# Performance work log

Measured on AMD Instinct MI355X. Metric: run time of the kernel, lower is better.

The kernel has to match this reference:

```python
import jax, jax.numpy as jnp
import numpy as np

DIM = 1024
B, S = 2, 2048

def _gelu(v):
    return jax.nn.gelu(v, approximate=False)

def setup_inputs() -> dict:
    key = jax.random.key(0)
    ks = jax.random.split(key, 24)
    d = DIM
    def lin(k, fan_in, fan_out):
        k1, k2 = jax.random.split(k)
        bound = 1.0 / np.sqrt(fan_in)
        W = jax.random.uniform(k1, (fan_in, fan_out), jnp.float32, -bound, bound)
        b = jax.random.uniform(k2, (fan_out,), jnp.float32, -bound, bound)
        return W, b
    w_pt1, b_pt1 = lin(ks[0], d, 2 * d)
    w_pt2, b_pt2 = lin(ks[1], 2 * d, d)
    w_wg, b_wg = lin(ks[2], d, d)
    w_mag, b_mag = lin(ks[3], d, d)
    w_q1, b_q1 = lin(ks[4], d, d)
    w_q2, b_q2 = lin(ks[5], d, d)
    w_mix, b_mix = lin(ks[6], d, 2 * d)
    w_o1, b_o1 = lin(ks[7], d, d)
    w_o2, b_o2 = lin(ks[8], d, d)
    return {
        "x": jax.random.normal(ks[9], (B, S, d), jnp.float32),
        "w_pt1": w_pt1, "b_pt1": b_pt1, "w_pt2": w_pt2, "b_pt2": b_pt2,
        "int_scale": jnp.ones((d,), jnp.float32) * 0.001,
        "w_wg": w_wg, "b_wg": b_wg,
        "gate_temp": jnp.ones((1,), jnp.float32) * 2.0,
        "w_mag": w_mag, "b_mag": b_mag,
        "w_q1": w_q1, "b_q1": b_q1, "w_q2": w_q2, "b_q2": b_q2,
        "w_mix": w_mix, "b_mix": b_mix,
        "ln_g": jnp.ones((d,), jnp.float32), "ln_b": jnp.zeros((d,), jnp.float32),
        "w_o1": w_o1, "b_o1": b_o1, "w_o2": w_o2, "b_o2": b_o2,
    }

def reference(x, w_pt1, b_pt1, w_pt2, b_pt2, int_scale, w_wg, b_wg, gate_temp,
              w_mag, b_mag, w_q1, b_q1, w_q2, b_q2, w_mix, b_mix,
              ln_g, ln_b, w_o1, b_o1, w_o2, b_o2):
    # input-dependent phase basis
    phase_delta = _gelu(x @ w_pt1 + b_pt1) @ w_pt2 + b_pt2          # [B,S,D]
    phi = jnp.cumsum(phase_delta * jnp.abs(int_scale), axis=1)
    # selective write gate + magnitude
    write_gate = jax.nn.sigmoid((x @ w_wg + b_wg) * gate_temp)
    magnitude = jax.nn.sigmoid(x @ w_mag + b_mag) * 5.0
    content = write_gate * x * magnitude
    # complex-phase memory accumulation (4 seq-length scans)
    memory_real = jnp.cumsum(content * jnp.cos(phi), axis=1)
    memory_imag = jnp.cumsum(content * jnp.sin(phi), axis=1)
    accum_weight = jnp.cumsum(write_gate * magnitude + 1e-8, axis=1)
    inv_s = 1.0 / jnp.sqrt(accum_weight)
    mr, mi = memory_real * inv_s, memory_imag * inv_s
    # query-phase retrieval (complex rotation)
    query_phase = phi + (_gelu(x @ w_q1 + b_q1) @ w_q2 + b_q2)
    cq, sq = jnp.cos(query_phase), jnp.sin(query_phase)
    retrieved_real = mr * cq + mi * sq
    retrieved_imag = mi * cq - mr * sq
    # input-dependent output mixing
    mix = x @ w_mix + b_mix
    d = x.shape[-1]
    mix_real = jax.nn.sigmoid(mix[..., :d])
    mix_imag = jax.nn.sigmoid(mix[..., d:])
    retrieved = mix_real * retrieved_real + mix_imag * retrieved_imag
    # output head: LayerNorm -> Linear -> GELU -> (Dropout=identity in eval) -> Linear
    mu = jnp.mean(retrieved, axis=-1, keepdims=True)
    var = jnp.var(retrieved, axis=-1, keepdims=True)
    ln = (retrieved - mu) / jnp.sqrt(var + 1e-5) * ln_g + ln_b
    out = _gelu(ln @ w_o1 + b_o1) @ w_o2 + b_o2
    return x + out
```

## Files before the change

### kernel.cpp

```cpp
#include <hip/hip_runtime.h>
#include <hip/hip_bf16.h>

#define MTOT 4096
#define DD   1024
#define D2   2048
#define SS   2048
#define BB   2
#define NC2  128
#define CL2  (SS/NC2)

typedef __attribute__((ext_vector_type(8))) short bf16x8;
typedef __attribute__((ext_vector_type(4))) float f32x4;

__device__ __forceinline__ float sigmf(float v){
    return 1.0f/(1.0f+__expf(-v));
}
__device__ __forceinline__ float geluf(float v){
    float u = 0.7978845608f*v*(1.0f + 0.044715f*v*v);
    float e = __expf(2.0f*u);
    float t = 1.0f - 2.0f/(e + 1.0f);
    return 0.5f*v*(1.0f + t);
}
__device__ __forceinline__ ushort f2bf(float f){
    unsigned u = __float_as_uint(f);
    unsigned r = (u + 0x7FFF + ((u>>16)&1)) >> 16;
    return (ushort)r;
}
__device__ __forceinline__ float bf2f(ushort u){
    return __uint_as_float(((unsigned)u)<<16);
}

__device__ __forceinline__ void stage_tile(
    const ushort* __restrict__ A, const ushort* __restrict__ Bt, int K,
    int m0, int n0, int k0, ushort* As, ushort* Bs)
{
    int tid = threadIdx.x;
    #pragma unroll
    for (int i = 0; i < 2; i++) {
        int e = (i*256 + tid) * 8;
        int r = e >> 5;
        int s = (e >> 3) & 3;
        int c = ((s ^ ((r >> 1) & 3)) << 3);
        __builtin_amdgcn_global_load_lds(
            (const __attribute__((address_space(1))) void*)(A + (size_t)(m0 + r)*K + k0 + c),
            (__attribute__((address_space(3))) void*)(As + e), 16, 0, 0);
        __builtin_amdgcn_global_load_lds(
            (const __attribute__((address_space(1))) void*)(Bt + (size_t)(n0 + r)*K + k0 + c),
            (__attribute__((address_space(3))) void*)(Bs + e), 16, 0, 0);
    }
}

__device__ __forceinline__ void load_frags(
    const ushort* As, const ushort* Bs, int wr, int wc, int lrow, int cs,
    bf16x8 (&af)[4], bf16x8 (&bfr)[4])
{
    #pragma unroll
    for (int i = 0; i < 4; i++) {
        int ra = wr*64 + i*16 + lrow;
        int rb = wc*64 + i*16 + lrow;
        af[i]  = *(const bf16x8*)(As + ra*32 + ((cs ^ ((ra>>1)&3))<<3));
        bfr[i] = *(const bf16x8*)(Bs + rb*32 + ((cs ^ ((rb>>1)&3))<<3));
    }
}

__device__ __forceinline__ void do_mfma(
    const bf16x8 (&af)[4], const bf16x8 (&bfr)[4], f32x4 (&acc)[4][4])
{
    __builtin_amdgcn_s_setprio(1);
    #pragma unroll
    for (int i = 0; i < 4; i++)
        #pragma unroll
        for (int j = 0; j < 4; j++)
            acc[i][j] = __builtin_amdgcn_mfma_f32_16x16x32_bf16(af[i], bfr[j], acc[i][j], 0, 0, 0);
    __builtin_amdgcn_s_setprio(0);
}

__device__ __forceinline__ void mgemm_core(
    const ushort* __restrict__ A, const ushort* __restrict__ Bt, int K,
    int m0, int n0, ushort (&As)[2][4096], ushort (&Bs)[2][4096], f32x4 (&acc)[4][4])
{
    int lane = threadIdx.x & 63, wave = threadIdx.x >> 6;
    int wr = wave >> 1, wc = wave & 1;
    int lrow = lane & 15, cs = lane >> 4;
    int NT = K >> 5;
    stage_tile(A, Bt, K, m0, n0, 0,  As[0], Bs[0]);
    stage_tile(A, Bt, K, m0, n0, 32, As[1], Bs[1]);
    for (int t = 0; t < NT-1; ++t) {
        asm volatile("s_waitcnt vmcnt(4)" ::: "memory");
        __builtin_amdgcn_s_barrier();
        bf16x8 af[4], bfr[4];
        load_frags(As[t&1], Bs[t&1], wr, wc, lrow, cs, af, bfr);
        if (t < NT-2) {
            asm volatile("s_waitcnt lgkmcnt(0)" ::: "memory");
            __builtin_amdgcn_s_barrier();
            stage_tile(A, Bt, K, m0, n0, (t+2) << 5, As[t&1], Bs[t&1]);
        }
        __builtin_amdgcn_sched_barrier(0);
        do_mfma(af, bfr, acc);
    }
    asm volatile("s_waitcnt vmcnt(0)" ::: "memory");
    __builtin_amdgcn_s_barrier();
    bf16x8 af[4], bfr[4];
    load_frags(As[(NT-1)&1], Bs[(NT-1)&1], wr, wc, lrow, cs, af, bfr);
    do_mfma(af, bfr, acc);
}

__global__ __launch_bounds__(256,4) void mgemmA_k(
    const ushort* __restrict__ xb, const ushort* __restrict__ Wt,
    const float* __restrict__ b_pt1, const float* __restrict__ b_wg,
    const float* __restrict__ b_mag, const float* __restrict__ b_q1,
    const float* __restrict__ b_mix, const float* __restrict__ gtemp,
    ushort* __restrict__ H1b, ushort* __restrict__ wgb, ushort* __restrict__ magb,
    ushort* __restrict__ Hqb, ushort* __restrict__ mixb)
{
    __shared__ ushort As[2][4096], Bs[2][4096];
    int bid = blockIdx.x;
    int xcd = bid & 7, local = bid >> 3;
    int m0 = (xcd*4 + (local & 3)) * 128;
    int n0 = (local >> 2) * 128;
    f32x4 acc[4][4] = {};
    mgemm_core(xb, Wt, 1024, m0, n0, As, Bs, acc);
    int lane = threadIdx.x & 63, wave = threadIdx.x >> 6;
    int wr = wave >> 1, wc = wave & 1;
    int rng = n0 >> 10;
    float gt = gtemp[0];
    #pragma unroll
    for (int i = 0; i < 4; i++) {
        int mb = m0 + wr*64 + i*16 + (lane>>4)*4;
        #pragma unroll
        for (int j = 0; j < 4; j++) {
            int n = n0 + wc*64 + j*16 + (lane&15);
            #pragma unroll
            for (int r = 0; r < 4; r++) {
                int m = mb + r;
                float v = acc[i][j][r];
                if (rng < 2) {
                    H1b[(size_t)m*D2 + n] = f2bf(geluf(v + b_pt1[n]));
                } else if (rng == 2) {
                    wgb[(size_t)m*DD + n-2048] = f2bf(sigmf((v + b_wg[n-2048])*gt));
                } else if (rng == 3) {
                    magb[(size_t)m*DD + n-3072] = f2bf(sigmf(v + b_mag[n-3072])*5.0f);
                } else if (rng == 4) {
                    Hqb[(size_t)m*DD + n-4096] = f2bf(geluf(v + b_q1[n-4096]));
                } else {
                    mixb[(size_t)m*D2 + n-5120] = f2bf(sigmf(v + b_mix[n-5120]));
                }
            }
        }
    }
}

__global__ __launch_bounds__(256,4) void mgemmBC_k(
    const ushort* __restrict__ H1b, const ushort* __restrict__ wt_pt2,
    const ushort* __restrict__ Hqb, const ushort* __restrict__ wt_q2,
    const float* __restrict__ b_pt2, const float* __restrict__ b_q2,
    const float* __restrict__ iscale,
    ushort* __restrict__ pdb, ushort* __restrict__ qadjb,
    float* __restrict__ csum_phi)
{
    __shared__ ushort As[2][4096], Bs[2][4096];
    int bid = blockIdx.x;
    int xcd = bid & 7, local = bid >> 3;
    int m0 = (xcd*4 + (local & 3)) * 128;
    int rest = local >> 2;
    int z = rest >> 3;
    int n0 = (rest & 7) * 128;
    const ushort* A  = z ? Hqb   : H1b;
    const ushort* Bt = z ? wt_q2 : wt_pt2;
    const float* bias = z ? b_q2 : b_pt2;
    int K = z ? 1024 : 2048;
    ushort* outp = z ? qadjb : pdb;
    f32x4 acc[4][4] = {};
    mgemm_core(A, Bt, K, m0, n0, As, Bs, acc);
    int lane = threadIdx.x & 63, wave = threadIdx.x >> 6;
    int wr = wave >> 1, wc = wave & 1;
    float csum_ij[4][4];
    #pragma unroll
    for (int i = 0; i < 4; i++) {
        int mb = m0 + wr*64 + i*16 + (lane>>4)*4;
        #pragma unroll
        for (int j = 0; j < 4; j++) {
            int n = n0 + wc*64 + j*16 + (lane&15);
            float bv = bias[n];
            float sc = z ? 1.0f : fabsf(iscale[n]);
            float s = 0.f;
            #pragma unroll
            for (int r = 0; r < 4; r++) {
                float v = acc[i][j][r] + bv;
                ushort bfv = f2bf(z ? v : v*sc);
                outp[(size_t)(mb+r)*DD + n] = bfv;
                s += bf2f(bfv);
            }
            csum_ij[i][j] = s;
        }
    }
    if (z == 0) {
        int b = m0 >> 11;
        int c0 = (m0 & 2047) >> 4;
        #pragma unroll
        for (int i = 0; i < 4; i++) {
            int c = c0 + wr*4 + i;
            #pragma unroll
            for (int j = 0; j < 4; j++) {
                float s = csum_ij[i][j];
                s += __shfl_xor(s, 16);
                s += __shfl_xor(s, 32);
                if ((lane >> 4) == 0) {
                    int n = n0 + wc*64 + j*16 + (lane&15);
                    csum_phi[((size_t)b*NC2 + c)*DD + n] = s;
                }
            }
        }
    }
}

template<int ACT, bool RESID, bool OUTBF16>
__global__ __launch_bounds__(256,4) void mgemm_k(
    const ushort* __restrict__ A, const ushort* __restrict__ Bt,
    const float* __restrict__ bias, const float* __restrict__ resid,
    void* __restrict__ Cout, int N, int K)
{
    __shared__ ushort As[2][4096], Bs[2][4096];
    int bid = blockIdx.x;
    int xcd = bid & 7, local = bid >> 3;
    int m0 = (xcd*4 + (local & 3)) * 128;
    int n0 = (local >> 2) * 128;
    f32x4 acc[4][4] = {};
    mgemm_core(A, Bt, K, m0, n0, As, Bs, acc);
    int lane = threadIdx.x & 63, wave = threadIdx.x >> 6;
    int wr = wave >> 1, wc = wave & 1;
    #pragma unroll
    for (int i = 0; i < 4; i++) {
        int mb = m0 + wr*64 + i*16 + (lane>>4)*4;
        #pragma unroll
        for (int j = 0; j < 4; j++) {
            int n = n0 + wc*64 + j*16 + (lane&15);
            float bv = bias[n];
            #pragma unroll
            for (int r = 0; r < 4; r++) {
                size_t idx = (size_t)(mb + r)*N + n;
                float v = acc[i][j][r] + bv;
                if (ACT==1) v = geluf(v);
                if (RESID) v += resid[idx];
                if (OUTBF16) ((ushort*)Cout)[idx] = f2bf(v);
                else         ((float*)Cout)[idx]  = v;
            }
        }
    }
}

__global__ __launch_bounds__(256) void cvt_bf16_k(const float* __restrict__ in, ushort* __restrict__ outp){
    size_t i = ((size_t)blockIdx.x*256 + threadIdx.x)*8;
    float4 a = *(const float4*)(in + i);
    float4 b = *(const float4*)(in + i + 4);
    ushort t[8];
    t[0]=f2bf(a.x); t[1]=f2bf(a.y); t[2]=f2bf(a.z); t[3]=f2bf(a.w);
    t[4]=f2bf(b.x); t[5]=f2bf(b.y); t[6]=f2bf(b.z); t[7]=f2bf(b.w);
    *(int4*)(outp + i) = *(const int4*)t;
}

__device__ __forceinline__ void tcvt_body(const float* W, ushort* Wt, int K, int N, int n0, int k0){
    __shared__ float tile[32][33];
    int tx = threadIdx.x & 7, ty = threadIdx.x >> 3;
    float4 v = *(const float4*)(W + (size_t)(k0+ty)*N + n0 + tx*4);
    tile[ty][tx*4+0]=v.x; tile[ty][tx*4+1]=v.y; tile[ty][tx*4+2]=v.z; tile[ty][tx*4+3]=v.w;
    __syncthreads();
    ushort t[4];
    #pragma unroll
    for (int i=0;i<4;i++) t[i] = f2bf(tile[tx*4+i][ty]);
    *(uint2*)(Wt + (size_t)(n0+ty)*K + k0 + tx*4) = *(const uint2*)t;
}

__global__ __launch_bounds__(256) void tcvt_all_k(
    const float* __restrict__ w_pt1, const float* __restrict__ w_mix,
    const float* __restrict__ w_wg,  const float* __restrict__ w_mag,
    const float* __restrict__ w_q1,  const float* __restrict__ w_q2,
    const float* __restrict__ w_o1,  const float* __restrict__ w_o2,
    const float* __restrict__ w_pt2,
    ushort* __restrict__ Wt_all, ushort* __restrict__ wt_q2,
    ushort* __restrict__ wt_o1,  ushort* __restrict__ wt_o2,
    ushort* __restrict__ wt_pt2)
{
    int bid = blockIdx.x;
    const float* W; ushort* Wt; int K, N, tile;
    if (bid < 2048)        { W=w_pt1; Wt=Wt_all;                      K=1024; N=2048; tile=bid; }
    else if (bid < 4096)   { W=w_mix; Wt=Wt_all+(size_t)5120*1024;    K=1024; N=2048; tile=bid-2048; }
    else if (bid < 5120)   { W=w_wg;  Wt=Wt_all+(size_t)2048*1024;    K=1024; N=1024; tile=bid-4096; }
    else if (bid < 6144)   { W=w_mag; Wt=Wt_all+(size_t)3072*1024;    K=1024; N=1024; tile=bid-5120; }
    else if (bid < 7168)   { W=w_q1;  Wt=Wt_all+(size_t)4096*1024;    K=1024; N=1024; tile=bid-6144; }
    else if (bid < 8192)   { W=w_q2;  Wt=wt_q2;                       K=1024; N=1024; tile=bid-7168; }
    else if (bid < 9216)   { W=w_o1;  Wt=wt_o1;                       K=1024; N=1024; tile=bid-8192; }
    else if (bid < 10240)  { W=w_o2;  Wt=wt_o2;                       K=1024; N=1024; tile=bid-9216; }
    else                   { W=w_pt2; Wt=wt_pt2;                      K=2048; N=1024; tile=bid-10240; }
    int nx = N >> 5;
    int n0 = (tile % nx) * 32, k0 = (tile / nx) * 32;
    tcvt_body(W, Wt, K, N, n0, k0);
}

__global__ void scan2_k(float* __restrict__ csum, int nchains){
    int idx = blockIdx.x*256 + threadIdx.x;
    if (idx >= nchains) return;
    int xg = idx / DD, d = idx % DD;
    float* p = csum + (size_t)xg*NC2*DD + d;
    float run = 0.f;
    for (int c = 0; c < NC2; c++){ float t = p[(size_t)c*DD]; p[(size_t)c*DD] = run; run += t; }
}

__global__ __launch_bounds__(256) void passB_k(
    const ushort* __restrict__ pdb, const ushort* __restrict__ wgb,
    const ushort* __restrict__ magb, const ushort* __restrict__ xb,
    const float* __restrict__ csum_phi, float* __restrict__ csum_tri)
{
    int d0 = (blockIdx.x*256 + threadIdx.x)*2;
    int c = blockIdx.y, b = blockIdx.z;
    size_t off = ((size_t)b*SS + (size_t)c*CL2)*DD + d0;
    float2 phv = *(const float2*)(csum_phi + ((size_t)b*NC2 + c)*DD + d0);
    float ph0 = phv.x, ph1 = phv.y;
    float a0=0.f, a1=0.f, b0=0.f, b1=0.f, c0=0.f, c1=0.f;
    for (int i = 0; i < CL2; i++){
        size_t o = off + (size_t)i*DD;
        ushort2 pdv = *(const ushort2*)(pdb + o);
        ushort2 wgv = *(const ushort2*)(wgb + o);
        ushort2 mgv = *(const ushort2*)(magb + o);
        ushort2 xv  = *(const ushort2*)(xb + o);
        ph0 += bf2f(pdv.x); ph1 += bf2f(pdv.y);
        float w0 = bf2f(wgv.x), w1 = bf2f(wgv.y);
        float m0 = bf2f(mgv.x), m1 = bf2f(mgv.y);
        float ct0 = w0*bf2f(xv.x)*m0, ct1 = w1*bf2f(xv.y)*m1;
        float sp0, cp0, sp1, cp1;
        sincosf(ph0, &sp0, &cp0); sincosf(ph1, &sp1, &cp1);
        a0 += ct0*cp0; a1 += ct1*cp1;
        b0 += ct0*sp0; b1 += ct1*sp1;
        c0 += fmaf(w0, m0, 1e-8f); c1 += fmaf(w1, m1, 1e-8f);
    }
    size_t cs = ((size_t)b*NC2 + c)*DD + d0;
    size_t G = (size_t)BB*NC2*DD;
    *(float2*)(csum_tri + cs)     = make_float2(a0, a1);
    *(float2*)(csum_tri + G+cs)   = make_float2(b0, b1);
    *(float2*)(csum_tri + 2*G+cs) = make_float2(c0, c1);
}

__global__ __launch_bounds__(256) void passC_k(
    const ushort* __restrict__ pdb, const ushort* __restrict__ wgb,
    const ushort* __restrict__ magb, const ushort* __restrict__ xb,
    const ushort* __restrict__ qadjb, const ushort* __restrict__ mixb,
    const float* __restrict__ csum_phi, const float* __restrict__ csum_tri,
    ushort* __restrict__ ret)
{
    int d0 = (blockIdx.x*256 + threadIdx.x)*2;
    int c = blockIdx.y, b = blockIdx.z;
    size_t off = ((size_t)b*SS + (size_t)c*CL2)*DD + d0;
    size_t cs = ((size_t)b*NC2 + c)*DD + d0;
    size_t G = (size_t)BB*NC2*DD;
    float2 phv = *(const float2*)(csum_phi + cs);
    float2 r0v = *(const float2*)(csum_tri + cs);
    float2 r1v = *(const float2*)(csum_tri + G+cs);
    float2 r2v = *(const float2*)(csum_tri + 2*G+cs);
    float ph0 = phv.x, ph1 = phv.y;
    float p0 = r0v.x, p1 = r0v.y, q0 = r1v.x, q1 = r1v.y, s0 = r2v.x, s1 = r2v.y;
    size_t row0 = (size_t)b*SS + (size_t)c*CL2;
    for (int i = 0; i < CL2; i++){
        size_t o = off + (size_t)i*DD;
        ushort2 pdv = *(const ushort2*)(pdb + o);
        ushort2 wgv = *(const ushort2*)(wgb + o);
        ushort2 mgv = *(const ushort2*)(magb + o);
        ushort2 xv  = *(const ushort2*)(xb + o);
        ushort2 qav = *(const ushort2*)(qadjb + o);
        size_t mb2 = (row0 + i)*D2 + d0;
        ushort2 mrv = *(const ushort2*)(mixb + mb2);
        ushort2 miv = *(const ushort2*)(mixb + mb2 + DD);
        ph0 += bf2f(pdv.x); ph1 += bf2f(pdv.y);
        float w0 = bf2f(wgv.x), w1 = bf2f(wgv.y);
        float m0 = bf2f(mgv.x), m1 = bf2f(mgv.y);
        float ct0 = w0*bf2f(xv.x)*m0, ct1 = w1*bf2f(xv.y)*m1;
        float sp0, cp0, sp1, cp1;
        sincosf(ph0, &sp0, &cp0); sincosf(ph1, &sp1, &cp1);
        p0 += ct0*cp0; p1 += ct1*cp1;
        q0 += ct0*sp0; q1 += ct1*sp1;
        s0 += fmaf(w0, m0, 1e-8f); s1 += fmaf(w1, m1, 1e-8f);
        float inv0 = rsqrtf(s0), inv1 = rsqrtf(s1);
        float mr0 = p0*inv0, mi0 = q0*inv0;
        float mr1 = p1*inv1, mi1 = q1*inv1;
        float sq0, cq0, sq1, cq1;
        sincosf(ph0 + bf2f(qav.x), &sq0, &cq0);
        sincosf(ph1 + bf2f(qav.y), &sq1, &cq1);
        float rr0 = mr0*cq0 + mi0*sq0, ri0 = mi0*cq0 - mr0*sq0;
        float rr1 = mr1*cq1 + mi1*sq1, ri1 = mi1*cq1 - mr1*sq1;
        ushort2 rv;
        rv.x = f2bf(bf2f(mrv.x)*rr0 + bf2f(miv.x)*ri0);
        rv.y = f2bf(bf2f(mrv.y)*rr1 + bf2f(miv.y)*ri1);
        *(ushort2*)(ret + o) = rv;
    }
}

__global__ __launch_bounds__(256) void ln_k(
    const ushort* __restrict__ ret, const float* __restrict__ ln_g,
    const float* __restrict__ ln_b, ushort* __restrict__ outp)
{
    int row = blockIdx.x;
    size_t base = (size_t)row*DD;
    int d0 = threadIdx.x*4;
    ushort4 rv = *(const ushort4*)(ret + base + d0);
    float v0 = bf2f(rv.x), v1 = bf2f(rv.y), v2 = bf2f(rv.z), v3 = bf2f(rv.w);
    float sum = v0+v1+v2+v3;
    float sumsq = v0*v0 + v1*v1 + v2*v2 + v3*v3;
    #pragma unroll
    for (int off=32; off; off>>=1){
        sum   += __shfl_down(sum,off);
        sumsq += __shfl_down(sumsq,off);
    }
    __shared__ float red[8];
    int lane = threadIdx.x & 63, wid = threadIdx.x >> 6;
    if (lane==0){ red[wid]=sum; red[4+wid]=sumsq; }
    __syncthreads();
    sum   = red[0]+red[1]+red[2]+red[3];
    sumsq = red[4]+red[5]+red[6]+red[7];
    float mu  = sum * (1.0f/DD);
    float var = sumsq*(1.0f/DD) - mu*mu;
    float rstd = rsqrtf(var + 1e-5f);
    float4 g = *(const float4*)(ln_g + d0);
    float4 bb = *(const float4*)(ln_b + d0);
    ushort4 ov;
    ov.x = f2bf((v0-mu)*rstd*g.x + bb.x);
    ov.y = f2bf((v1-mu)*rstd*g.y + bb.y);
    ov.z = f2bf((v2-mu)*rstd*g.z + bb.z);
    ov.w = f2bf((v3-mu)*rstd*g.w + bb.w);
    *(ushort4*)(outp + base + d0) = ov;
}

extern "C" void kernel_launch(void* const* d_in, const int* in_sizes, int n_in,
                              void* d_out, int out_size, void* d_ws, size_t ws_size,
                              hipStream_t stream)
{
    const float* x     = (const float*)d_in[0];
    const float* w_pt1 = (const float*)d_in[1];
    const float* b_pt1 = (const float*)d_in[2];
    const float* w_pt2 = (const float*)d_in[3];
    const float* b_pt2 = (const float*)d_in[4];
    const float* iscale= (const float*)d_in[5];
    const float* w_wg  = (const float*)d_in[6];
    const float* b_wg  = (const float*)d_in[7];
    const float* gtemp = (const float*)d_in[8];
    const float* w_mag = (const float*)d_in[9];
    const float* b_mag = (const float*)d_in[10];
    const float* w_q1  = (const float*)d_in[11];
    const float* b_q1  = (const float*)d_in[12];
    const float* w_q2  = (const float*)d_in[13];
    const float* b_q2  = (const float*)d_in[14];
    const float* w_mix = (const float*)d_in[15];
    const float* b_mix = (const float*)d_in[16];
    const float* ln_g  = (const float*)d_in[17];
    const float* ln_b  = (const float*)d_in[18];
    const float* w_o1  = (const float*)d_in[19];
    const float* b_o1  = (const float*)d_in[20];
    const float* w_o2  = (const float*)d_in[21];
    const float* b_o2  = (const float*)d_in[22];
    float* out = (float*)d_out;

    const size_t SZ = (size_t)MTOT*DD;
    ushort* u = (ushort*)d_ws;
    ushort* xb    = u;                 u += SZ;
    ushort* H1b   = u;                 u += 2*SZ;
    ushort* ret   = H1b;
    ushort* Hqb   = u;                 u += SZ;
    ushort* lnb   = Hqb;
    ushort* wgb   = u;                 u += SZ;
    ushort* magb  = u;                 u += SZ;
    ushort* mixb  = u;                 u += 2*SZ;
    ushort* Hob   = u;                 u += SZ;
    ushort* pdb   = u;                 u += SZ;
    ushort* qadjb = u;                 u += SZ;
    ushort* Wt_all= u;                 u += (size_t)7168*1024;
    ushort* wt_pt2= u;                 u += (size_t)1024*2048;
    ushort* wt_q2 = u;                 u += (size_t)1024*1024;
    ushort* wt_o1 = u;                 u += (size_t)1024*1024;
    ushort* wt_o2 = u;                 u += (size_t)1024*1024;
    float* csum_phi = (float*)u;
    float* csum_tri = csum_phi + (size_t)BB*NC2*DD;

    dim3 blk(256);
    cvt_bf16_k<<<dim3(SZ/2048), blk, 0, stream>>>(x, xb);
    tcvt_all_k<<<dim3(12288), blk, 0, stream>>>(w_pt1, w_mix, w_wg, w_mag, w_q1, w_q2,
                                                w_o1, w_o2, w_pt2,
                                                Wt_all, wt_q2, wt_o1, wt_o2, wt_pt2);
    mgemmA_k<<<dim3(1792), blk, 0, stream>>>(xb, Wt_all, b_pt1, b_wg, b_mag, b_q1, b_mix,
                                             gtemp, H1b, wgb, magb, Hqb, mixb);
    mgemmBC_k<<<dim3(512), blk, 0, stream>>>(H1b, wt_pt2, Hqb, wt_q2, b_pt2, b_q2,
                                             iscale, pdb, qadjb, csum_phi);
    scan2_k<<<dim3((BB*DD+255)/256), blk, 0, stream>>>(csum_phi, BB*DD);
    passB_k<<<dim3(DD/512, NC2, BB), blk, 0, stream>>>(pdb, wgb, magb, xb, csum_phi, csum_tri);
    scan2_k<<<dim3((3*BB*DD+255)/256), blk, 0, stream>>>(csum_tri, 3*BB*DD);
    passC_k<<<dim3(DD/512, NC2, BB), blk, 0, stream>>>(pdb, wgb, magb, xb, qadjb, mixb,
                                                       csum_phi, csum_tri, ret);
    ln_k<<<dim3(MTOT), blk, 0, stream>>>(ret, ln_g, ln_b, lnb);
    mgemm_k<1,false,true><<<dim3(256), blk, 0, stream>>>(lnb, wt_o1, b_o1, nullptr, Hob, DD, DD);
    mgemm_k<0,true,false><<<dim3(256), blk, 0, stream>>>(Hob, wt_o2, b_o2, x, out, DD, DD);
}
```

Baseline: 240.0 us.

## Triple-buffer GEMM LDS staging and fuse input cast into weight conversion

The shared GEMM core moves from a double-buffered to a triple-buffered LDS pipeline, so each tile is prefetched three steps ahead and global-load latency is hidden better. Launch bounds drop from 4 to 3 blocks per CU to fit the extra 16 KB of LDS per block. The x-to-bf16 cast is folded into the weight transpose-convert kernel as extra blocks, removing one launch, and the chunk-scan loop gets an unroll pragma. The trade-off is lower occupancy for a deeper prefetch.

```diff
diff --git a/kernel.cpp b/kernel.cpp
--- a/kernel.cpp
+++ b/kernel.cpp
@@ -77,7 +77,7 @@
 
 __device__ __forceinline__ void mgemm_core(
     const ushort* __restrict__ A, const ushort* __restrict__ Bt, int K,
-    int m0, int n0, ushort (&As)[2][4096], ushort (&Bs)[2][4096], f32x4 (&acc)[4][4])
+    int m0, int n0, ushort (&As)[3][4096], ushort (&Bs)[3][4096], f32x4 (&acc)[4][4])
 {
     int lane = threadIdx.x & 63, wave = threadIdx.x >> 6;
     int wr = wave >> 1, wc = wave & 1;
@@ -85,27 +85,39 @@
     int NT = K >> 5;
     stage_tile(A, Bt, K, m0, n0, 0,  As[0], Bs[0]);
     stage_tile(A, Bt, K, m0, n0, 32, As[1], Bs[1]);
-    for (int t = 0; t < NT-1; ++t) {
+    stage_tile(A, Bt, K, m0, n0, 64, As[2], Bs[2]);
+    int bi = 0;
+    for (int t = 0; t < NT-2; ++t) {
+        asm volatile("s_waitcnt vmcnt(8)" ::: "memory");
+        __builtin_amdgcn_s_barrier();
+        bf16x8 af[4], bfr[4];
+        load_frags(As[bi], Bs[bi], wr, wc, lrow, cs, af, bfr);
+        asm volatile("s_waitcnt lgkmcnt(0)" ::: "memory");
+        __builtin_amdgcn_s_barrier();
+        if (t < NT-3)
+            stage_tile(A, Bt, K, m0, n0, (t+3) << 5, As[bi], Bs[bi]);
+        __builtin_amdgcn_sched_barrier(0);
+        do_mfma(af, bfr, acc);
+        bi = (bi == 2) ? 0 : bi + 1;
+    }
+    {
         asm volatile("s_waitcnt vmcnt(4)" ::: "memory");
         __builtin_amdgcn_s_barrier();
         bf16x8 af[4], bfr[4];
-        load_frags(As[t&1], Bs[t&1], wr, wc, lrow, cs, af, bfr);
-        if (t < NT-2) {
-            asm volatile("s_waitcnt lgkmcnt(0)" ::: "memory");
-            __builtin_amdgcn_s_barrier();
-            stage_tile(A, Bt, K, m0, n0, (t+2) << 5, As[t&1], Bs[t&1]);
-        }
-        __builtin_amdgcn_sched_barrier(0);
+        load_frags(As[bi], Bs[bi], wr, wc, lrow, cs, af, bfr);
         do_mfma(af, bfr, acc);
-    }
-    asm volatile("s_waitcnt vmcnt(0)" ::: "memory");
-    __builtin_amdgcn_s_barrier();
-    bf16x8 af[4], bfr[4];
-    load_frags(As[(NT-1)&1], Bs[(NT-1)&1], wr, wc, lrow, cs, af, bfr);
-    do_mfma(af, bfr, acc);
-}
-
-__global__ __launch_bounds__(256,4) void mgemmA_k(
+        bi = (bi == 2) ? 0 : bi + 1;
+    }
+    {
+        asm volatile("s_waitcnt vmcnt(0)" ::: "memory");
+        __builtin_amdgcn_s_barrier();
+        bf16x8 af[4], bfr[4];
+        load_frags(As[bi], Bs[bi], wr, wc, lrow, cs, af, bfr);
+        do_mfma(af, bfr, acc);
+    }
+}
+
+__global__ __launch_bounds__(256,3) void mgemmA_k(
     const ushort* __restrict__ xb, const ushort* __restrict__ Wt,
     const float* __restrict__ b_pt1, const float* __restrict__ b_wg,
     const float* __restrict__ b_mag, const float* __restrict__ b_q1,
@@ -113,7 +125,7 @@
     ushort* __restrict__ H1b, ushort* __restrict__ wgb, ushort* __restrict__ magb,
     ushort* __restrict__ Hqb, ushort* __restrict__ mixb)
 {
-    __shared__ ushort As[2][4096], Bs[2][4096];
+    __shared__ ushort As[3][4096], Bs[3][4096];
     int bid = blockIdx.x;
     int xcd = bid & 7, local = bid >> 3;
     int m0 = (xcd*4 + (local & 3)) * 128;
@@ -150,7 +162,7 @@
     }
 }
 
-__global__ __launch_bounds__(256,4) void mgemmBC_k(
+__global__ __launch_bounds__(256,3) void mgemmBC_k(
     const ushort* __restrict__ H1b, const ushort* __restrict__ wt_pt2,
     const ushort* __restrict__ Hqb, const ushort* __restrict__ wt_q2,
     const float* __restrict__ b_pt2, const float* __restrict__ b_q2,
@@ -158,7 +170,7 @@
     ushort* __restrict__ pdb, ushort* __restrict__ qadjb,
     float* __restrict__ csum_phi)
 {
-    __shared__ ushort As[2][4096], Bs[2][4096];
+    __shared__ ushort As[3][4096], Bs[3][4096];
     int bid = blockIdx.x;
     int xcd = bid & 7, local = bid >> 3;
     int m0 = (xcd*4 + (local & 3)) * 128;
@@ -215,12 +227,12 @@
 }
 
 template<int ACT, bool RESID, bool OUTBF16>
-__global__ __launch_bounds__(256,4) void mgemm_k(
+__global__ __launch_bounds__(256,3) void mgemm_k(
     const ushort* __restrict__ A, const ushort* __restrict__ Bt,
     const float* __restrict__ bias, const float* __restrict__ resid,
     void* __restrict__ Cout, int N, int K)
 {
-    __shared__ ushort As[2][4096], Bs[2][4096];
+    __shared__ ushort As[3][4096], Bs[3][4096];
     int bid = blockIdx.x;
     int xcd = bid & 7, local = bid >> 3;
     int m0 = (xcd*4 + (local & 3)) * 128;
@@ -249,16 +261,6 @@
     }
 }
 
-__global__ __launch_bounds__(256) void cvt_bf16_k(const float* __restrict__ in, ushort* __restrict__ outp){
-    size_t i = ((size_t)blockIdx.x*256 + threadIdx.x)*8;
-    float4 a = *(const float4*)(in + i);
-    float4 b = *(const float4*)(in + i + 4);
-    ushort t[8];
-    t[0]=f2bf(a.x); t[1]=f2bf(a.y); t[2]=f2bf(a.z); t[3]=f2bf(a.w);
-    t[4]=f2bf(b.x); t[5]=f2bf(b.y); t[6]=f2bf(b.z); t[7]=f2bf(b.w);
-    *(int4*)(outp + i) = *(const int4*)t;
-}
-
 __device__ __forceinline__ void tcvt_body(const float* W, ushort* Wt, int K, int N, int n0, int k0){
     __shared__ float tile[32][33];
     int tx = threadIdx.x & 7, ty = threadIdx.x >> 3;
@@ -271,17 +273,27 @@
     *(uint2*)(Wt + (size_t)(n0+ty)*K + k0 + tx*4) = *(const uint2*)t;
 }
 
-__global__ __launch_bounds__(256) void tcvt_all_k(
+__global__ __launch_bounds__(256) void cvt_all_k(
     const float* __restrict__ w_pt1, const float* __restrict__ w_mix,
     const float* __restrict__ w_wg,  const float* __restrict__ w_mag,
     const float* __restrict__ w_q1,  const float* __restrict__ w_q2,
     const float* __restrict__ w_o1,  const float* __restrict__ w_o2,
-    const float* __restrict__ w_pt2,
+    const float* __restrict__ w_pt2, const float* __restrict__ x,
     ushort* __restrict__ Wt_all, ushort* __restrict__ wt_q2,
     ushort* __restrict__ wt_o1,  ushort* __restrict__ wt_o2,
-    ushort* __restrict__ wt_pt2)
+    ushort* __restrict__ wt_pt2, ushort* __restrict__ xb)
 {
     int bid = blockIdx.x;
+    if (bid >= 12288) {
+        size_t i = ((size_t)(bid - 12288)*256 + threadIdx.x)*8;
+        float4 a = *(const float4*)(x + i);
+        float4 b = *(const float4*)(x + i + 4);
+        ushort t[8];
+        t[0]=f2bf(a.x); t[1]=f2bf(a.y); t[2]=f2bf(a.z); t[3]=f2bf(a.w);
+        t[4]=f2bf(b.x); t[5]=f2bf(b.y); t[6]=f2bf(b.z); t[7]=f2bf(b.w);
+        *(int4*)(xb + i) = *(const int4*)t;
+        return;
+    }
     const float* W; ushort* Wt; int K, N, tile;
     if (bid < 2048)        { W=w_pt1; Wt=Wt_all;                      K=1024; N=2048; tile=bid; }
     else if (bid < 4096)   { W=w_mix; Wt=Wt_all+(size_t)5120*1024;    K=1024; N=2048; tile=bid-2048; }
@@ -303,6 +315,7 @@
     int xg = idx / DD, d = idx % DD;
     float* p = csum + (size_t)xg*NC2*DD + d;
     float run = 0.f;
+    #pragma unroll 4
     for (int c = 0; c < NC2; c++){ float t = p[(size_t)c*DD]; p[(size_t)c*DD] = run; run += t; }
 }
 
@@ -479,10 +492,9 @@
     float* csum_tri = csum_phi + (size_t)BB*NC2*DD;
 
     dim3 blk(256);
-    cvt_bf16_k<<<dim3(SZ/2048), blk, 0, stream>>>(x, xb);
-    tcvt_all_k<<<dim3(12288), blk, 0, stream>>>(w_pt1, w_mix, w_wg, w_mag, w_q1, w_q2,
-                                                w_o1, w_o2, w_pt2,
-                                                Wt_all, wt_q2, wt_o1, wt_o2, wt_pt2);
+    cvt_all_k<<<dim3(14336), blk, 0, stream>>>(w_pt1, w_mix, w_wg, w_mag, w_q1, w_q2,
+                                               w_o1, w_o2, w_pt2, x,
+                                               Wt_all, wt_q2, wt_o1, wt_o2, wt_pt2, xb);
     mgemmA_k<<<dim3(1792), blk, 0, stream>>>(xb, Wt_all, b_pt1, b_wg, b_mag, b_q1, b_mix,
                                              gtemp, H1b, wgb, magb, Hqb, mixb);
     mgemmBC_k<<<dim3(512), blk, 0, stream>>>(H1b, wt_pt2, Hqb, wt_q2, b_pt2, b_q2,
```

Measured after the change: 269.0 us. 1.12x slower.
